# Optimization experiments

Hardware: AMD Instinct MI355X
Metric: run time of the kernel (lower is better)

The kernel has to match this reference:

```python
import jax, jax.numpy as jnp
import numpy as np

N, E, G = 50000, 200000, 1000
EPS = 1e-5
NEG_SLOPE = 0.2


def setup_inputs() -> dict:
    key = jax.random.key(0)
    ks = jax.random.split(key, 24)
    p = lambda k, shape: jax.random.normal(k, shape, jnp.float32) * 0.05
    inp = {
        "x": jax.random.normal(ks[0], (N, 64), jnp.float32),
        "edge_index": jax.random.randint(ks[1], (2, E), 0, N, jnp.int32),
        "batch": jnp.sort(jax.random.randint(ks[2], (N,), 0, G, jnp.int32)),
        "solvent_fingerprint": jax.random.uniform(ks[3], (G, 128), jnp.float32),
        # GAT layer 1: 64 -> 4 heads x 128
        "W1": p(ks[4], (64, 512)), "a1_src": p(ks[5], (4, 128)), "a1_dst": p(ks[6], (4, 128)), "b1": jnp.zeros((512,), jnp.float32),
        "bn1_g": jnp.ones((512,), jnp.float32), "bn1_b": jnp.zeros((512,), jnp.float32),
        # GAT layer 2: 512 -> 4 heads x 256
        "W2": p(ks[7], (512, 1024)), "a2_src": p(ks[8], (4, 256)), "a2_dst": p(ks[9], (4, 256)), "b2": jnp.zeros((1024,), jnp.float32),
        "bn2_g": jnp.ones((1024,), jnp.float32), "bn2_b": jnp.zeros((1024,), jnp.float32),
        # GCN: 1024 -> 256
        "Wg": p(ks[10], (1024, 256)), "bg": jnp.zeros((256,), jnp.float32),
        "bn3_g": jnp.ones((256,), jnp.float32), "bn3_b": jnp.zeros((256,), jnp.float32),
        # MLP head
        "Ws": p(ks[11], (128, 128)), "bs": jnp.zeros((128,), jnp.float32),
        "Wf1": p(ks[12], (640, 128)), "bf1": jnp.zeros((128,), jnp.float32),
        "bnf_g": jnp.ones((128,), jnp.float32), "bnf_b": jnp.zeros((128,), jnp.float32),
        "Wf2": p(ks[13], (128, 1)), "bf2": jnp.zeros((1,), jnp.float32),
    }
    return inp


def _batchnorm(x, g, b):
    mu = x.mean(0)
    var = x.var(0)
    return (x - mu) * jax.lax.rsqrt(var + EPS) * g + b


def _gat(x, src, dst, W, a_src, a_dst, b, H, C):
    n = x.shape[0]
    h = (x @ W).reshape(n, H, C)                      # [N,H,C]
    al_s = (h * a_src).sum(-1)                        # [N,H]
    al_d = (h * a_dst).sum(-1)                        # [N,H]
    e = jax.nn.leaky_relu(al_s[src] + al_d[dst], NEG_SLOPE)   # [E,H]
    m = jax.ops.segment_max(e, dst, num_segments=n)
    ex = jnp.exp(e - m[dst])
    s = jax.ops.segment_sum(ex, dst, num_segments=n)
    alpha = ex / jnp.maximum(s[dst], 1e-16)
    out = jax.ops.segment_sum(h[src] * alpha[..., None], dst, num_segments=n)  # [N,H,C]
    return out.reshape(n, H * C) + b


def _gcn(x, src, dst, W, b):
    n = x.shape[0]
    h = x @ W
    deg = jax.ops.segment_sum(jnp.ones_like(dst, jnp.float32), dst, num_segments=n)
    dinv = jax.lax.rsqrt(jnp.maximum(deg, 1.0))
    norm = dinv[src] * dinv[dst]
    return jax.ops.segment_sum(h[src] * norm[:, None], dst, num_segments=n) + b


def reference(x, edge_index, batch, solvent_fingerprint,
              W1, a1_src, a1_dst, b1, bn1_g, bn1_b,
              W2, a2_src, a2_dst, b2, bn2_g, bn2_b,
              Wg, bg, bn3_g, bn3_b,
              Ws, bs, Wf1, bf1, bnf_g, bnf_b, Wf2, bf2):
    n = x.shape[0]
    loops = jnp.arange(n, dtype=edge_index.dtype)
    src = jnp.concatenate([edge_index[0], loops])
    dst = jnp.concatenate([edge_index[1], loops])

    h = _gat(x, src, dst, W1, a1_src, a1_dst, b1, 4, 128)
    h = jax.nn.relu(_batchnorm(h, bn1_g, bn1_b))
    h = _gat(h, src, dst, W2, a2_src, a2_dst, b2, 4, 256)
    h = jax.nn.relu(_batchnorm(h, bn2_g, bn2_b))
    h = _gcn(h, src, dst, Wg, bg)
    h = jax.nn.relu(_batchnorm(h, bn3_g, bn3_b))

    cnt = jax.ops.segment_sum(jnp.ones((n,), jnp.float32), batch, num_segments=G)
    gap = jax.ops.segment_sum(h, batch, num_segments=G) / jnp.maximum(cnt, 1.0)[:, None]
    gmp = jax.ops.segment_max(h, batch, num_segments=G)
    gmp = jnp.where(jnp.isfinite(gmp), gmp, 0.0)

    solv = jax.nn.relu(solvent_fingerprint @ Ws + bs)
    z = jnp.concatenate([gap, gmp, solv], axis=1)          # [G,640]
    z = jax.nn.relu(_batchnorm(z @ Wf1 + bf1, bnf_g, bnf_b))
    # dropout: identity in eval/deterministic reference
    return jax.nn.sigmoid(z @ Wf2 + bf2)
```

## Files before the change

### kernel.cpp

```cpp
#include <hip/hip_runtime.h>
#include <cmath>

#define LEAK 0.2f
#define BN_EPS 1e-5f

static inline int cdiv(long long a, long long b){ return (int)((a + b - 1) / b); }

typedef __attribute__((ext_vector_type(8))) short bf16x8;
typedef __attribute__((ext_vector_type(4))) float f32x4;

__device__ __forceinline__ float bf2f(unsigned short u){
    return __uint_as_float(((unsigned int)u) << 16);
}
__device__ __forceinline__ unsigned short f2bf(float f){
    unsigned int u = __float_as_uint(f);
    u += 0x7FFFu + ((u >> 16) & 1u);
    return (unsigned short)(u >> 16);
}
__device__ __forceinline__ float edge_ex(float s, float d){
    float t = s + d;
    t = (t >= 0.f) ? t : LEAK * t;
    return __expf(t);
}

#define GLOAD_LDS16(gsrc, ldst) \
    __builtin_amdgcn_global_load_lds( \
        (const __attribute__((address_space(1))) unsigned int*)(gsrc), \
        (__attribute__((address_space(3))) unsigned int*)(ldst), 16, 0, 0)

__global__ __launch_bounds__(256) void gemm_mfma(
    const unsigned short* __restrict__ A, const unsigned short* __restrict__ Bt,
    unsigned short* __restrict__ D, int M, int K, int lda, int ldb, int ldc,
    int NX, int NYT, float* __restrict__ ps, float* __restrict__ pq, int Dbn,
    int axoff)
{
    const int id = blockIdx.x;
    const int xcd = id & 7;
    const int j = id >> 3;
    const int bx = j % NX;
    const int by = (j / NX) * 8 + xcd;
    if (by >= NYT) return;

    __shared__ unsigned short As[128 * 64];
    __shared__ unsigned short Bs[128 * 64];
    const int t = threadIdx.x;
    const int row0 = by * 128, col0 = bx * 128;
    const int lane = t & 63, wv = t >> 6;
    const int wm = (wv >> 1) << 6, wn = (wv & 1) << 6;
    const int lm = lane & 15, lq = lane >> 4;

    const unsigned short* Ab = A + (size_t)bx * axoff;
    const int sr  = t >> 3;
    const int scs = (t & 7) << 3;
    const int gsw = (((t & 7) ^ (sr & 7)) << 3);
    const unsigned short* ap[4];
    const unsigned short* bp[4];
    unsigned short* la[4];
    unsigned short* lb[4];
    #pragma unroll
    for (int q = 0; q < 4; ++q) {
        int r = sr + q * 32;
        int gra = row0 + r; if (gra >= M) gra = M - 1;
        ap[q] = Ab + (size_t)gra * lda + gsw;
        bp[q] = Bt + (size_t)(col0 + r) * ldb + gsw;
        la[q] = &As[r * 64 + scs];
        lb[q] = &Bs[r * 64 + scs];
    }

    f32x4 acc[4][4] = {};
    const int rx = lm & 7;

    for (int k0 = 0; k0 < K; k0 += 64) {
        #pragma unroll
        for (int q = 0; q < 4; ++q) {
            GLOAD_LDS16(ap[q] + k0, la[q]);
            GLOAD_LDS16(bp[q] + k0, lb[q]);
        }
        __syncthreads();

        #pragma unroll
        for (int kk = 0; kk < 2; ++kk) {
            const int ck = (((kk << 2) + lq) ^ rx) << 3;
            bf16x8 af[4], bfr[4];
            #pragma unroll
            for (int mi = 0; mi < 4; ++mi)
                af[mi] = *(const bf16x8*)&As[(wm + mi * 16 + lm) * 64 + ck];
            #pragma unroll
            for (int ni = 0; ni < 4; ++ni)
                bfr[ni] = *(const bf16x8*)&Bs[(wn + ni * 16 + lm) * 64 + ck];
            #pragma unroll
            for (int mi = 0; mi < 4; ++mi)
                #pragma unroll
                for (int ni = 0; ni < 4; ++ni)
                    acc[mi][ni] = __builtin_amdgcn_mfma_f32_16x16x32_bf16(
                        af[mi], bfr[ni], acc[mi][ni], 0, 0, 0);
        }
        __syncthreads();
    }

    #pragma unroll
    for (int mi = 0; mi < 4; ++mi) {
        #pragma unroll
        for (int r = 0; r < 4; ++r) {
            int row = wm + mi * 16 + lq * 4 + r;
            unsigned short* base = (row < 64) ? &As[row * 128] : &Bs[(row - 64) * 128];
            #pragma unroll
            for (int ni = 0; ni < 4; ++ni) {
                int col = (wn + ni * 16 + lm) ^ (lq << 4);
                base[col] = f2bf(acc[mi][ni][r]);
            }
        }
    }
    __syncthreads();
    #pragma unroll
    for (int i = 0; i < 8; ++i) {
        int idx = i * 256 + t;
        int row = idx >> 4;
        int lqr = (row >> 2) & 3;
        int c8l = (idx & 15) << 3;
        int c8p = c8l ^ (lqr << 4);
        int grow = row0 + row;
        if (grow < M) {
            const unsigned short* base = (row < 64) ? &As[row * 128] : &Bs[(row - 64) * 128];
            bf16x8 v = *(const bf16x8*)&base[c8p];
            *(bf16x8*)(D + (size_t)grow * ldc + col0 + c8l) = v;
        }
    }

    if (ps) {
        float cs[4] = {}, cq[4] = {};
        #pragma unroll
        for (int mi = 0; mi < 4; ++mi) {
            int row_b = row0 + wm + mi * 16 + lq * 4;
            #pragma unroll
            for (int ni = 0; ni < 4; ++ni)
                #pragma unroll
                for (int r = 0; r < 4; ++r)
                    if (row_b + r < M) {
                        float v = acc[mi][ni][r];
                        cs[ni] += v; cq[ni] += v * v;
                    }
        }
        #pragma unroll
        for (int ni = 0; ni < 4; ++ni) {
            cs[ni] += __shfl_xor(cs[ni], 16); cs[ni] += __shfl_xor(cs[ni], 32);
            cq[ni] += __shfl_xor(cq[ni], 16); cq[ni] += __shfl_xor(cq[ni], 32);
        }
        if (lane < 16) {
            size_t slot = (size_t)(blockIdx.x & 255) * Dbn + col0;
            #pragma unroll
            for (int ni = 0; ni < 4; ++ni) {
                int c = wn + ni * 16 + lane;
                atomicAdd(&ps[slot + c], cs[ni]);
                atomicAdd(&pq[slot + c], cq[ni]);
            }
        }
    }
}

__global__ __launch_bounds__(256) void logits_valu(
    const unsigned short* __restrict__ A, const unsigned short* __restrict__ vat,
    float* __restrict__ C, int M, int K)
{
    __shared__ unsigned short vs[8 * 512];
    const int t = threadIdx.x;
    for (int i = t; i < K; i += 256)
        *(bf16x8*)&vs[i * 8] = *(const bf16x8*)(vat + (size_t)i * 8);
    __syncthreads();

    const int lane = t & 63;
    const int w = blockIdx.x * 4 + (t >> 6);
    const int Gl = K >> 3;
    const int rpw = 64 / Gl;
    const int sub = lane / Gl;
    const int li = lane - sub * Gl;
    long long row = (long long)w * rpw + sub;
    if (row >= M) return;

    bf16x8 hv = *(const bf16x8*)(A + row * K + li * 8);
    float hf[8];
    #pragma unroll
    for (int j = 0; j < 8; ++j) hf[j] = bf2f((unsigned short)hv[j]);

    float s[8];
    #pragma unroll
    for (int o = 0; o < 8; ++o) {
        bf16x8 v = *(const bf16x8*)&vs[o * K + li * 8];
        float acc = 0.f;
        #pragma unroll
        for (int j = 0; j < 8; ++j) acc += hf[j] * bf2f((unsigned short)v[j]);
        s[o] = acc;
    }
    for (int off = Gl >> 1; off; off >>= 1) {
        #pragma unroll
        for (int o = 0; o < 8; ++o) s[o] += __shfl_xor(s[o], off);
    }
    #pragma unroll
    for (int o = 0; o < 8; ++o)
        if (li == o) C[row * 8 + o] = s[o];
}

__global__ __launch_bounds__(256) void bn_apply_logits512(
    const unsigned short* __restrict__ g1b,
    const float* __restrict__ scale, const float* __restrict__ shift,
    const unsigned short* __restrict__ vat,
    unsigned short* __restrict__ o1n, float* __restrict__ C, int M, int nblk)
{
    __shared__ unsigned short vs[8 * 512];
    const int t = threadIdx.x;
    for (int i = t; i < 512; i += 256)
        *(bf16x8*)&vs[i * 8] = *(const bf16x8*)(vat + (size_t)i * 8);
    __syncthreads();

    const int lane = t & 63;
    const long long stride = (long long)nblk * 4;
    for (long long row = (long long)blockIdx.x * 4 + (t >> 6); row < M; row += stride) {
        bf16x8 u = *(const bf16x8*)(g1b + row * 512 + lane * 8);
        float4 sc0 = *(const float4*)(scale + lane * 8);
        float4 sc1 = *(const float4*)(scale + lane * 8 + 4);
        float4 sh0 = *(const float4*)(shift + lane * 8);
        float4 sh1 = *(const float4*)(shift + lane * 8 + 4);
        float hf[8];
        hf[0] = fmaxf(bf2f((unsigned short)u[0]) * sc0.x + sh0.x, 0.f);
        hf[1] = fmaxf(bf2f((unsigned short)u[1]) * sc0.y + sh0.y, 0.f);
        hf[2] = fmaxf(bf2f((unsigned short)u[2]) * sc0.z + sh0.z, 0.f);
        hf[3] = fmaxf(bf2f((unsigned short)u[3]) * sc0.w + sh0.w, 0.f);
        hf[4] = fmaxf(bf2f((unsigned short)u[4]) * sc1.x + sh1.x, 0.f);
        hf[5] = fmaxf(bf2f((unsigned short)u[5]) * sc1.y + sh1.y, 0.f);
        hf[6] = fmaxf(bf2f((unsigned short)u[6]) * sc1.z + sh1.z, 0.f);
        hf[7] = fmaxf(bf2f((unsigned short)u[7]) * sc1.w + sh1.w, 0.f);
        bf16x8 o;
        #pragma unroll
        for (int j = 0; j < 8; ++j) o[j] = (short)f2bf(hf[j]);
        *(bf16x8*)(o1n + row * 512 + lane * 8) = o;

        float s[8];
        #pragma unroll
        for (int oo = 0; oo < 8; ++oo) {
            bf16x8 v = *(const bf16x8*)&vs[oo * 512 + lane * 8];
            float acc = 0.f;
            #pragma unroll
            for (int j = 0; j < 8; ++j) acc += hf[j] * bf2f((unsigned short)v[j]);
            s[oo] = acc;
        }
        #pragma unroll
        for (int off = 32; off; off >>= 1) {
            #pragma unroll
            for (int oo = 0; oo < 8; ++oo) s[oo] += __shfl_xor(s[oo], off);
        }
        #pragma unroll
        for (int oo = 0; oo < 8; ++oo)
            if (lane == oo) C[row * 8 + oo] = s[oo];
    }
}

__global__ __launch_bounds__(256) void prep_all(
    const float* __restrict__ W1, const float* __restrict__ W2,
    const float* __restrict__ Wg, const float* __restrict__ x,
    const float* __restrict__ a1s, const float* __restrict__ a1d,
    const float* __restrict__ a2s, const float* __restrict__ a2d,
    const int* __restrict__ batch,
    unsigned short* __restrict__ W1ct, unsigned short* __restrict__ W2t,
    unsigned short* __restrict__ Wgt, unsigned short* __restrict__ xb,
    unsigned short* __restrict__ vat1, unsigned short* __restrict__ vat2,
    int* __restrict__ cursor, int* __restrict__ gptr,
    int N, int G_,
    int c0, int c1, int c2, int c3, int c4, int c5, int c6)
{
    const int t = threadIdx.x;
    const int bid = blockIdx.x;
    if (bid < c0) {
        int i = bid * 256 + t;
        int o = i >> 6, k = i & 63;
        W1ct[i] = f2bf(W1[(size_t)k * 512 + o]);
    } else if (bid < c1) {
        int i = (bid - c0) * 256 + t;
        int k = i >> 10, n = i & 1023;
        W2t[(size_t)n * 512 + k] = f2bf(W2[i]);
    } else if (bid < c2) {
        int i = (bid - c1) * 256 + t;
        int k = i >> 8, n = i & 255;
        Wgt[(size_t)n * 1024 + k] = f2bf(Wg[i]);
    } else if (bid < c3) {
        int i = (bid - c2) * 256 + t;
        if (i < N * 16) {
            float4 v = *reinterpret_cast<const float4*>(x + (size_t)i * 4);
            ushort4 o = { f2bf(v.x), f2bf(v.y), f2bf(v.z), f2bf(v.w) };
            *reinterpret_cast<ushort4*>(xb + (size_t)i * 4) = o;
        }
    } else if (bid < c4) {
        int w = (((bid - c3) * 256 + t) >> 6);
        int lane = t & 63;
        int k = w >> 2, h = w & 3;
        const float* wp = W1 + (size_t)k * 512 + h * 128;
        const float* as = a1s + h * 128;
        const float* ad = a1d + h * 128;
        float s = 0.f, d = 0.f;
        for (int c = lane; c < 128; c += 64) {
            float v = wp[c];
            s += v * as[c];
            d += v * ad[c];
        }
        #pragma unroll
        for (int off = 32; off; off >>= 1) {
            s += __shfl_down(s, off);
            d += __shfl_down(d, off);
        }
        if (lane == 0) {
            vat1[(size_t)h * 64 + k] = f2bf(s);
            vat1[(size_t)(4 + h) * 64 + k] = f2bf(d);
        }
    } else if (bid < c5) {
        int w = (((bid - c4) * 256 + t) >> 6);
        int lane = t & 63;
        int k = w >> 2, h = w & 3;
        const float* wp = W2 + (size_t)k * 1024 + h * 256;
        const float* as = a2s + h * 256;
        const float* ad = a2d + h * 256;
        float s = 0.f, d = 0.f;
        for (int c = lane; c < 256; c += 64) {
            float v = wp[c];
            s += v * as[c];
            d += v * ad[c];
        }
        #pragma unroll
        for (int off = 32; off; off >>= 1) {
            s += __shfl_down(s, off);
            d += __shfl_down(d, off);
        }
        if (lane == 0) {
            vat2[(size_t)h * 512 + k] = f2bf(s);
            vat2[(size_t)(4 + h) * 512 + k] = f2bf(d);
        }
    } else if (bid < c6) {
        int i = (bid - c5) * 256 + t;
        if (i < N) cursor[i] = 1;
    } else {
        int g = (bid - c6) * 256 + t;
        if (g > G_) return;
        if (g == G_) { gptr[G_] = N; return; }
        int lo = 0, hi = N;
        while (lo < hi) { int mid = (lo + hi) >> 1; if (batch[mid] < g) lo = mid + 1; else hi = mid; }
        gptr[g] = lo;
    }
}

template<bool RELU>
__global__ __launch_bounds__(256) void gemm_small(
    const float* __restrict__ A, const float* __restrict__ B,
    const float* __restrict__ bias, float* __restrict__ C,
    int M, int K, int lda, int ldb, int ldc,
    float* __restrict__ ps, float* __restrict__ pq)
{
    __shared__ float As[2][640];
    const int t = threadIdx.x;
    const int r = t >> 7, c = t & 127;
    const int row0 = blockIdx.x * 2;
    for (int i = t; i < 2 * K; i += 256) {
        int rr = i / K, kk = i - rr * K;
        int gr = row0 + rr;
        As[rr][kk] = (gr < M) ? A[(size_t)gr * lda + kk] : 0.f;
    }
    __syncthreads();
    float acc0 = 0.f, acc1 = 0.f;
    for (int k = 0; k < K; k += 8) {
        float4 a0 = *reinterpret_cast<const float4*>(&As[r][k]);
        float4 a1 = *reinterpret_cast<const float4*>(&As[r][k + 4]);
        acc0 += a0.x * B[(size_t)(k + 0) * ldb + c];
        acc1 += a0.y * B[(size_t)(k + 1) * ldb + c];
        acc0 += a0.z * B[(size_t)(k + 2) * ldb + c];
        acc1 += a0.w * B[(size_t)(k + 3) * ldb + c];
        acc0 += a1.x * B[(size_t)(k + 4) * ldb + c];
        acc1 += a1.y * B[(size_t)(k + 5) * ldb + c];
        acc0 += a1.z * B[(size_t)(k + 6) * ldb + c];
        acc1 += a1.w * B[(size_t)(k + 7) * ldb + c];
    }
    int row = row0 + r;
    if (row < M) {
        float v = acc0 + acc1;
        if (bias) v += bias[c];
        if (RELU) v = fmaxf(v, 0.f);
        C[(size_t)row * ldc + c] = v;
        if (ps) {
            size_t slot = (size_t)(blockIdx.x & 255) * 128 + c;
            atomicAdd(&ps[slot], v);
            atomicAdd(&pq[slot], v * v);
        }
    }
}

__device__ __forceinline__ int e_src(const int* es, int E, int k){ return k < E ? es[k] : k - E; }
__device__ __forceinline__ int e_dst(const int* ed, int E, int k){ return k < E ? ed[k] : k - E; }

__global__ void hist_dst(const int* __restrict__ ed, int E, int* __restrict__ cnt)
{
    int k = blockIdx.x * blockDim.x + threadIdx.x;
    if (k < E) atomicAdd(&cnt[ed[k]], 1);
}

__global__ __launch_bounds__(256) void scan_blk(const int* __restrict__ cnt,
                                                int* __restrict__ rowptr,
                                                int* __restrict__ bsums, int n)
{
    __shared__ int ts[256];
    const int t = threadIdx.x;
    const int i0 = blockIdx.x * 1024 + t * 4;
    int4 v = {0, 0, 0, 0};
    if (i0 + 3 < n) v = *reinterpret_cast<const int4*>(cnt + i0);
    else {
        if (i0 + 0 < n) v.x = cnt[i0 + 0];
        if (i0 + 1 < n) v.y = cnt[i0 + 1];
        if (i0 + 2 < n) v.z = cnt[i0 + 2];
        if (i0 + 3 < n) v.w = cnt[i0 + 3];
    }
    int lsum = v.x + v.y + v.z + v.w;
    ts[t] = lsum;
    __syncthreads();
    #pragma unroll
    for (int off = 1; off < 256; off <<= 1) {
        int u = (t >= off) ? ts[t - off] : 0;
        __syncthreads();
        ts[t] += u;
        __syncthreads();
    }
    int excl = ts[t] - lsum;
    if (i0 + 0 < n) rowptr[i0 + 0] = excl;
    if (i0 + 1 < n) rowptr[i0 + 1] = excl + v.x;
    if (i0 + 2 < n) rowptr[i0 + 2] = excl + v.x + v.y;
    if (i0 + 3 < n) rowptr[i0 + 3] = excl + v.x + v.y + v.z;
    if (t == 255) bsums[blockIdx.x] = ts[255];
}

__global__ __launch_bounds__(256) void scan_tops(int* __restrict__ bsums,
                                                 int* __restrict__ rowptr, int nb, int n)
{
    __shared__ int ts[256];
    const int t = threadIdx.x;
    int v = (t < nb) ? bsums[t] : 0;
    ts[t] = v;
    __syncthreads();
    #pragma unroll
    for (int off = 1; off < 256; off <<= 1) {
        int u = (t >= off) ? ts[t - off] : 0;
        __syncthreads();
        ts[t] += u;
        __syncthreads();
    }
    if (t < nb) bsums[t] = ts[t] - v;
    if (t == 255) rowptr[n] = ts[255];
}

__global__ void scan_add(int* __restrict__ rowptr, int* __restrict__ cursor,
                         const int* __restrict__ bsums, int n)
{
    int i = blockIdx.x * blockDim.x + threadIdx.x;
    if (i >= n) return;
    int r = rowptr[i] + bsums[i >> 10];
    rowptr[i] = r;
    cursor[i] = r;
}

__global__ void csr_scatter_dinv(const int* __restrict__ es, const int* __restrict__ ed,
                                 int E, int Etot, int* __restrict__ cursor,
                                 int* __restrict__ col,
                                 const int* __restrict__ rowptr,
                                 float* __restrict__ dinv, int N, int NBsc)
{
    const int bid = blockIdx.x;
    const int t = threadIdx.x;
    if (bid < NBsc) {
        int k = bid * 256 + t;
        if (k >= Etot) return;
        int sn = e_src(es, E, k), dn = e_dst(ed, E, k);
        int pos = atomicAdd(&cursor[dn], 1);
        col[pos] = sn;
    } else {
        int i = (bid - NBsc) * 256 + t;
        if (i < N) dinv[i] = rsqrtf(fmaxf((float)(rowptr[i + 1] - rowptr[i]), 1.f));
    }
}

__global__ void gat_agg4_64(const int* __restrict__ rowptr, const int* __restrict__ col,
                            const unsigned short* __restrict__ xb,
                            const float* __restrict__ alsd,
                            unsigned short* __restrict__ agg, int N)
{
    int w = (int)(((long long)blockIdx.x * blockDim.x + threadIdx.x) >> 6);
    int lane = threadIdx.x & 63;
    if (w >= N) return;
    float4 dt = *reinterpret_cast<const float4*>(alsd + (size_t)w * 8 + 4);
    int r0 = rowptr[w], r1 = rowptr[w + 1];
    float a0 = 0.f, a1 = 0.f, a2 = 0.f, a3 = 0.f;
    float s0 = 0.f, s1 = 0.f, s2 = 0.f, s3 = 0.f;
    int e = r0;
    for (; e + 1 < r1; e += 2) {
        int snA = col[e], snB = col[e + 1];
        float4 stA = *reinterpret_cast<const float4*>(alsd + (size_t)snA * 8);
        float4 stB = *reinterpret_cast<const float4*>(alsd + (size_t)snB * 8);
        float xA = bf2f(xb[(size_t)snA * 64 + lane]);
        float xB = bf2f(xb[(size_t)snB * 64 + lane]);
        float eA0 = edge_ex(stA.x, dt.x), eB0 = edge_ex(stB.x, dt.x);
        float eA1 = edge_ex(stA.y, dt.y), eB1 = edge_ex(stB.y, dt.y);
        float eA2 = edge_ex(stA.z, dt.z), eB2 = edge_ex(stB.z, dt.z);
        float eA3 = edge_ex(stA.w, dt.w), eB3 = edge_ex(stB.w, dt.w);
        a0 += eA0 * xA + eB0 * xB;  s0 += eA0 + eB0;
        a1 += eA1 * xA + eB1 * xB;  s1 += eA1 + eB1;
        a2 += eA2 * xA + eB2 * xB;  s2 += eA2 + eB2;
        a3 += eA3 * xA + eB3 * xB;  s3 += eA3 + eB3;
    }
    if (e < r1) {
        int sn = col[e];
        float4 st = *reinterpret_cast<const float4*>(alsd + (size_t)sn * 8);
        float xA = bf2f(xb[(size_t)sn * 64 + lane]);
        float e0 = edge_ex(st.x, dt.x);
        float e1 = edge_ex(st.y, dt.y);
        float e2 = edge_ex(st.z, dt.z);
        float e3 = edge_ex(st.w, dt.w);
        a0 += e0 * xA; s0 += e0;
        a1 += e1 * xA; s1 += e1;
        a2 += e2 * xA; s2 += e2;
        a3 += e3 * xA; s3 += e3;
    }
    unsigned short* op = agg + (size_t)w * 256 + lane;
    op[0]   = f2bf(a0 / fmaxf(s0, 1e-16f));
    op[64]  = f2bf(a1 / fmaxf(s1, 1e-16f));
    op[128] = f2bf(a2 / fmaxf(s2, 1e-16f));
    op[192] = f2bf(a3 / fmaxf(s3, 1e-16f));
}

__global__ __launch_bounds__(256) void gat_gather512_ex(
    const int* __restrict__ rowptr, const int* __restrict__ col,
    const unsigned short* __restrict__ h, int ldh,
    const float* __restrict__ alsd, int pr,
    unsigned short* __restrict__ out,
    float* __restrict__ ps, float* __restrict__ pq, int N)
{
    const int t = threadIdx.x;
    const int lane = t & 63;
    const int wv = t >> 6;
    int w = (int)(((long long)blockIdx.x * 256 + t) >> 6);
    const bool valid = (w < N);

    float v0=0.f,v1=0.f,v2=0.f,v3=0.f;
    float u0=0.f,u1=0.f,u2=0.f,u3=0.f;
    if (valid) {
        float2 dt = *reinterpret_cast<const float2*>(alsd + (size_t)w * 8 + 4 + 2 * pr);
        int r0 = rowptr[w], r1 = rowptr[w + 1];
        float s0 = 0.f, s1 = 0.f;
        float a00=0.f,a01=0.f,a02=0.f,a03=0.f;
        float a10=0.f,a11=0.f,a12=0.f,a13=0.f;
        int e = r0;
        for (; e + 1 < r1; e += 2) {
            int snA = col[e], snB = col[e + 1];
            float2 stA = *reinterpret_cast<const float2*>(alsd + (size_t)snA * 8 + 2 * pr);
            float2 stB = *reinterpret_cast<const float2*>(alsd + (size_t)snB * 8 + 2 * pr);
            const unsigned short* pA = h + (size_t)snA * ldh + lane * 4;
            const unsigned short* pB = h + (size_t)snB * ldh + lane * 4;
            ushort4 hA0 = *reinterpret_cast<const ushort4*>(pA);
            ushort4 hA1 = *reinterpret_cast<const ushort4*>(pA + 256);
            ushort4 hB0 = *reinterpret_cast<const ushort4*>(pB);
            ushort4 hB1 = *reinterpret_cast<const ushort4*>(pB + 256);
            float eA0 = edge_ex(stA.x, dt.x), eB0 = edge_ex(stB.x, dt.x);
            float eA1 = edge_ex(stA.y, dt.y), eB1 = edge_ex(stB.y, dt.y);
            s0 += eA0 + eB0; s1 += eA1 + eB1;
            a00 += bf2f(hA0.x) * eA0 + bf2f(hB0.x) * eB0;
            a01 += bf2f(hA0.y) * eA0 + bf2f(hB0.y) * eB0;
            a02 += bf2f(hA0.z) * eA0 + bf2f(hB0.z) * eB0;
            a03 += bf2f(hA0.w) * eA0 + bf2f(hB0.w) * eB0;
            a10 += bf2f(hA1.x) * eA1 + bf2f(hB1.x) * eB1;
            a11 += bf2f(hA1.y) * eA1 + bf2f(hB1.y) * eB1;
            a12 += bf2f(hA1.z) * eA1 + bf2f(hB1.z) * eB1;
            a13 += bf2f(hA1.w) * eA1 + bf2f(hB1.w) * eB1;
        }
        if (e < r1) {
            int sn = col[e];
            float2 st = *reinterpret_cast<const float2*>(alsd + (size_t)sn * 8 + 2 * pr);
            float e0 = edge_ex(st.x, dt.x);
            float e1 = edge_ex(st.y, dt.y);
            const unsigned short* p = h + (size_t)sn * ldh + lane * 4;
            ushort4 h0 = *reinterpret_cast<const ushort4*>(p);
            ushort4 h1 = *reinterpret_cast<const ushort4*>(p + 256);
            s0 += e0; s1 += e1;
            a00 += bf2f(h0.x) * e0; a01 += bf2f(h0.y) * e0;
            a02 += bf2f(h0.z) * e0; a03 += bf2f(h0.w) * e0;
            a10 += bf2f(h1.x) * e1; a11 += bf2f(h1.y) * e1;
            a12 += bf2f(h1.z) * e1; a13 += bf2f(h1.w) * e1;
        }
        float i0 = 1.f / fmaxf(s0, 1e-16f);
        float i1 = 1.f / fmaxf(s1, 1e-16f);
        v0 = a00*i0; v1 = a01*i0; v2 = a02*i0; v3 = a03*i0;
        u0 = a10*i1; u1 = a11*i1; u2 = a12*i1; u3 = a13*i1;
        ushort4 o0 = { f2bf(v0), f2bf(v1), f2bf(v2), f2bf(v3) };
        ushort4 o1 = { f2bf(u0), f2bf(u1), f2bf(u2), f2bf(u3) };
        unsigned short* op = out + (size_t)w * 512 + lane * 4;
        *reinterpret_cast<ushort4*>(op)       = o0;
        *reinterpret_cast<ushort4*>(op + 256) = o1;
    }

    __shared__ float ls[4][512];
    __shared__ float lq[4][512];
    int c0 = lane * 4;
    ls[wv][c0+0]=v0; ls[wv][c0+1]=v1; ls[wv][c0+2]=v2; ls[wv][c0+3]=v3;
    ls[wv][256+c0+0]=u0; ls[wv][256+c0+1]=u1; ls[wv][256+c0+2]=u2; ls[wv][256+c0+3]=u3;
    lq[wv][c0+0]=v0*v0; lq[wv][c0+1]=v1*v1; lq[wv][c0+2]=v2*v2; lq[wv][c0+3]=v3*v3;
    lq[wv][256+c0+0]=u0*u0; lq[wv][256+c0+1]=u1*u1; lq[wv][256+c0+2]=u2*u2; lq[wv][256+c0+3]=u3*u3;
    __syncthreads();
    const size_t slot = (size_t)(blockIdx.x & 255) * 512;
    #pragma unroll
    for (int c = t; c < 512; c += 256) {
        float s = ls[0][c] + ls[1][c] + ls[2][c] + ls[3][c];
        float q = lq[0][c] + lq[1][c] + lq[2][c] + lq[3][c];
        atomicAdd(&ps[slot + c], s);
        atomicAdd(&pq[slot + c], q);
    }
}

__global__ __launch_bounds__(256) void gcn_gather256(
    const int* __restrict__ rowptr, const int* __restrict__ col,
    const unsigned short* __restrict__ h,
    const float* __restrict__ dinv,
    unsigned short* __restrict__ out,
    float* __restrict__ ps, float* __restrict__ pq, int N)
{
    const int t = threadIdx.x;
    const int lane = t & 63;
    const int wv = t >> 6;
    int w = (int)(((long long)blockIdx.x * 256 + t) >> 6);
    const bool valid = (w < N);

    float v0=0.f,v1=0.f,v2=0.f,v3=0.f;
    if (valid) {
        int r0 = rowptr[w], r1 = rowptr[w + 1];
        float a0 = 0.f, a1 = 0.f, a2 = 0.f, a3 = 0.f;
        int e = r0;
        for (; e + 1 < r1; e += 2) {
            int sn0 = col[e], sn1 = col[e + 1];
            float w0 = dinv[sn0], w1 = dinv[sn1];
            ushort4 hv0 = *reinterpret_cast<const ushort4*>(h + (size_t)sn0 * 256 + lane * 4);
            ushort4 hv1 = *reinterpret_cast<const ushort4*>(h + (size_t)sn1 * 256 + lane * 4);
            a0 += bf2f(hv0.x) * w0 + bf2f(hv1.x) * w1;
            a1 += bf2f(hv0.y) * w0 + bf2f(hv1.y) * w1;
            a2 += bf2f(hv0.z) * w0 + bf2f(hv1.z) * w1;
            a3 += bf2f(hv0.w) * w0 + bf2f(hv1.w) * w1;
        }
        if (e < r1) {
            int sn = col[e];
            float wv2 = dinv[sn];
            ushort4 hv = *reinterpret_cast<const ushort4*>(h + (size_t)sn * 256 + lane * 4);
            a0 += bf2f(hv.x) * wv2; a1 += bf2f(hv.y) * wv2;
            a2 += bf2f(hv.z) * wv2; a3 += bf2f(hv.w) * wv2;
        }
        float dn = dinv[w];
        v0 = a0 * dn; v1 = a1 * dn; v2 = a2 * dn; v3 = a3 * dn;
        ushort4 o = { f2bf(v0), f2bf(v1), f2bf(v2), f2bf(v3) };
        *reinterpret_cast<ushort4*>(out + (size_t)w * 256 + lane * 4) = o;
    }

    __shared__ float ls[4][256];
    __shared__ float lq[4][256];
    int c0 = lane * 4;
    ls[wv][c0+0]=v0; ls[wv][c0+1]=v1; ls[wv][c0+2]=v2; ls[wv][c0+3]=v3;
    lq[wv][c0+0]=v0*v0; lq[wv][c0+1]=v1*v1; lq[wv][c0+2]=v2*v2; lq[wv][c0+3]=v3*v3;
    __syncthreads();
    const size_t slot = (size_t)(blockIdx.x & 255) * 256;
    if (t < 256) {
        int c = t;
        float s = ls[0][c] + ls[1][c] + ls[2][c] + ls[3][c];
        float q = lq[0][c] + lq[1][c] + lq[2][c] + lq[3][c];
        atomicAdd(&ps[slot + c], s);
        atomicAdd(&pq[slot + c], q);
    }
}

template<int D>
__global__ __launch_bounds__(256) void bn_reduce_fin(
    const float* __restrict__ ps, const float* __restrict__ pq,
    const float* __restrict__ g, const float* __restrict__ b,
    float* __restrict__ scale, float* __restrict__ shift, int Y, float invM)
{
    const int t = threadIdx.x;
    const int cl = t & 63;
    const int c = blockIdx.x * 64 + cl;
    const int ph = t >> 6;
    float s = 0.f, q = 0.f;
    for (int y = ph; y < Y; y += 4) {
        s += ps[(size_t)y * D + c];
        q += pq[(size_t)y * D + c];
    }
    __shared__ float ls[4][64];
    __shared__ float lq[4][64];
    ls[ph][cl] = s; lq[ph][cl] = q;
    __syncthreads();
    if (ph == 0) {
        s = ls[0][cl] + ls[1][cl] + ls[2][cl] + ls[3][cl];
        q = lq[0][cl] + lq[1][cl] + lq[2][cl] + lq[3][cl];
        float mu = s * invM;
        float var = q * invM - mu * mu;
        float rs = rsqrtf(var + BN_EPS) * g[c];
        scale[c] = rs;
        shift[c] = b[c] - mu * rs;
    }
}

__global__ void bn_apply_bfbf(const unsigned short* __restrict__ x,
                              const float* __restrict__ scale, const float* __restrict__ shift,
                              unsigned short* __restrict__ dst, int total4, int Cb4,
                              int ldx, int ldd)
{
    int i = blockIdx.x * blockDim.x + threadIdx.x;
    if (i >= total4) return;
    int r = i / Cb4, c4 = (i - r * Cb4) * 4;
    ushort4 u = *reinterpret_cast<const ushort4*>(x + (size_t)r * ldx + c4);
    float4 sc = *reinterpret_cast<const float4*>(scale + c4);
    float4 sh = *reinterpret_cast<const float4*>(shift + c4);
    ushort4 o;
    o.x = f2bf(fmaxf(bf2f(u.x) * sc.x + sh.x, 0.f));
    o.y = f2bf(fmaxf(bf2f(u.y) * sc.y + sh.y, 0.f));
    o.z = f2bf(fmaxf(bf2f(u.z) * sc.z + sh.z, 0.f));
    o.w = f2bf(fmaxf(bf2f(u.w) * sc.w + sh.w, 0.f));
    *reinterpret_cast<ushort4*>(dst + (size_t)r * ldd + c4) = o;
}

__global__ __launch_bounds__(256) void pool_solv(
    const unsigned short* __restrict__ h,
    const float* __restrict__ scale, const float* __restrict__ shift,
    const int* __restrict__ gptr, float* __restrict__ z, int G_,
    const float* __restrict__ sfp, const float* __restrict__ Wsm,
    const float* __restrict__ bsm)
{
    __shared__ float As[2][640];
    const int t = threadIdx.x;
    const int bid = blockIdx.x;
    if (bid < G_) {
        int g = bid;
        int c = t;
        int r0 = gptr[g], r1 = gptr[g + 1];
        float sc = scale[c], sh = shift[c];
        float s = 0.f, m = 0.f;
        int i = r0;
        for (; i + 1 < r1; i += 2) {
            float v0 = fmaxf(bf2f(h[(size_t)i * 256 + c]) * sc + sh, 0.f);
            float v1 = fmaxf(bf2f(h[(size_t)(i + 1) * 256 + c]) * sc + sh, 0.f);
            s += v0 + v1;
            m = fmaxf(m, fmaxf(v0, v1));
        }
        if (i < r1) {
            float v = fmaxf(bf2f(h[(size_t)i * 256 + c]) * sc + sh, 0.f);
            s += v;
            m = fmaxf(m, v);
        }
        float cnt = fmaxf((float)(r1 - r0), 1.f);
        z[(size_t)g * 640 + c] = s / cnt;
        z[(size_t)g * 640 + 256 + c] = m;
    } else {
        const int r = t >> 7, c = t & 127;
        const int row0 = (bid - G_) * 2;
        for (int i = t; i < 256; i += 256) {
            int rr = i >> 7, kk = i & 127;
            int gr = row0 + rr;
            As[rr][kk] = (gr < G_) ? sfp[(size_t)gr * 128 + kk] : 0.f;
        }
        __syncthreads();
        float acc0 = 0.f, acc1 = 0.f;
        for (int k = 0; k < 128; k += 8) {
            float4 a0 = *reinterpret_cast<const float4*>(&As[r][k]);
            float4 a1 = *reinterpret_cast<const float4*>(&As[r][k + 4]);
            acc0 += a0.x * Wsm[(size_t)(k + 0) * 128 + c];
            acc1 += a0.y * Wsm[(size_t)(k + 1) * 128 + c];
            acc0 += a0.z * Wsm[(size_t)(k + 2) * 128 + c];
            acc1 += a0.w * Wsm[(size_t)(k + 3) * 128 + c];
            acc0 += a1.x * Wsm[(size_t)(k + 4) * 128 + c];
            acc1 += a1.y * Wsm[(size_t)(k + 5) * 128 + c];
            acc0 += a1.z * Wsm[(size_t)(k + 6) * 128 + c];
            acc1 += a1.w * Wsm[(size_t)(k + 7) * 128 + c];
        }
        int row = row0 + r;
        if (row < G_) {
            float v = fmaxf(acc0 + acc1 + bsm[c], 0.f);
            z[(size_t)row * 640 + 512 + c] = v;
        }
    }
}

__global__ void final_head_bn(const float* __restrict__ f1,
                              const float* __restrict__ scale, const float* __restrict__ shift,
                              const float* __restrict__ Wf2, const float* __restrict__ bf2,
                              float* __restrict__ out, int G_)
{
    int w = (int)(((long long)blockIdx.x * blockDim.x + threadIdx.x) >> 6);
    int lane = threadIdx.x & 63;
    if (w >= G_) return;
    float s = 0.f;
    #pragma unroll
    for (int q = 0; q < 2; ++q) {
        int c = lane + q * 64;
        float v = fmaxf(f1[(size_t)w * 128 + c] * scale[c] + shift[c], 0.f);
        s += v * Wf2[c];
    }
    #pragma unroll
    for (int off = 32; off; off >>= 1) s += __shfl_down(s, off);
    if (lane == 0) out[w] = 1.f / (1.f + __expf(-(s + bf2[0])));
}

__global__ void sentinel(float* __restrict__ out, int n, float v)
{
    int i = blockIdx.x * blockDim.x + threadIdx.x;
    if (i < n) out[i] = v;
}

extern "C" void kernel_launch(void* const* d_in, const int* in_sizes, int n_in,
                              void* d_out, int out_size, void* d_ws, size_t ws_size,
                              hipStream_t stream)
{
    const float* x    = (const float*)d_in[0];
    const int*   ei   = (const int*)d_in[1];
    const int*   batch= (const int*)d_in[2];
    const float* sfp  = (const float*)d_in[3];
    const float* W1   = (const float*)d_in[4];
    const float* a1s  = (const float*)d_in[5];
    const float* a1d  = (const float*)d_in[6];
    const float* bn1g = (const float*)d_in[8];
    const float* bn1b = (const float*)d_in[9];
    const float* W2   = (const float*)d_in[10];
    const float* a2s  = (const float*)d_in[11];
    const float* a2d  = (const float*)d_in[12];
    const float* bn2g = (const float*)d_in[14];
    const float* bn2b = (const float*)d_in[15];
    const float* Wg   = (const float*)d_in[16];
    const float* bn3g = (const float*)d_in[18];
    const float* bn3b = (const float*)d_in[19];
    const float* Wsm  = (const float*)d_in[20];
    const float* bsm  = (const float*)d_in[21];
    const float* Wf1  = (const float*)d_in[22];
    const float* bnfg = (const float*)d_in[24];
    const float* bnfb = (const float*)d_in[25];
    const float* Wf2  = (const float*)d_in[26];
    const float* bf2  = (const float*)d_in[27];
    float* outp = (float*)d_out;

    const int N    = in_sizes[0] / 64;
    const int E    = in_sizes[1] / 2;
    const int G_   = in_sizes[3] / 128;
    const int Etot = E + N;
    const int* esrc = ei;
    const int* edst = ei + E;
    const int YB = 256;
    const int NB = cdiv(N, 1024);
    const int NYT = cdiv(N, 128);
    const int NYT8 = cdiv(NYT, 8) * 8;

    float* ws = (float*)d_ws;
    size_t off = 0;
    float* accA  = ws + off; off += (size_t)N * 256;
    float* h3acc = ws + off; off += (size_t)N * 256;
    unsigned short* g1b   = (unsigned short*)accA;
    unsigned short* g3b   = (unsigned short*)accA;
    unsigned short* h2all = (unsigned short*)accA;
    unsigned short* R1 = (unsigned short*)(ws + off); off += (size_t)N * 256;
    unsigned short* o1n = R1;
    unsigned short* hb  = (unsigned short*)(ws + off); off += (size_t)N * 128;
    unsigned short* xb  = (unsigned short*)(ws + off); off += (size_t)N * 32;
    float* alsd = ws + off; off += (size_t)N * 8;
    float* dinv = ws + off; off += N;
    float* bsc = ws + off; off += 1024;
    float* bsh = ws + off; off += 1024;
    float* ps  = ws + off; off += (size_t)YB * 1920;
    float* pq  = ws + off; off += (size_t)YB * 1920;
    float* psP0 = ps + (size_t)YB * 512;
    float* psP1 = ps + (size_t)YB * 1024;
    float* psG  = ps + (size_t)YB * 1536;
    float* psF  = ps + (size_t)YB * 1792;
    float* pqP0 = pq + (size_t)YB * 512;
    float* pqP1 = pq + (size_t)YB * 1024;
    float* pqG  = pq + (size_t)YB * 1536;
    float* pqF  = pq + (size_t)YB * 1792;
    float* z   = ws + off; off += (size_t)G_ * 640;
    float* f1  = ws + off; off += (size_t)G_ * 128;
    int* rowptr = (int*)(ws + off); off += (size_t)(N + 1);
    int* colc   = (int*)(ws + off); off += (size_t)Etot;
    int* gptr   = (int*)(ws + off); off += (size_t)(G_ + 1);
    int* bsums  = (int*)(ws + off); off += 256;
    off = (off + 3) & ~(size_t)3;
    unsigned short* vat1 = (unsigned short*)(ws + off); off += 128 * 64 / 2;
    unsigned short* vat2 = (unsigned short*)(ws + off); off += 128 * 512 / 2;
    unsigned short* W1ct = (unsigned short*)(ws + off); off += 512 * 64 / 2;
    unsigned short* W2t = (unsigned short*)(ws + off); off += 512 * 1024 / 2;
    unsigned short* Wgt = (unsigned short*)(ws + off); off += 1024 * 256 / 2;
    int* cursor = (int*)alsd;
    size_t need = off * 4;
    if (ws_size < need) {
        sentinel<<<cdiv(out_size, 256), 256, 0, stream>>>(outp, out_size, (float)(ws_size >> 20));
        return;
    }

    const int BLK = 256;
    dim3 blk(BLK);

    hipMemsetAsync(ps, 0, (size_t)YB * 1920 * 4, stream);
    hipMemsetAsync(pq, 0, (size_t)YB * 1920 * 4, stream);

    const int c0 = 128;
    const int c1 = c0 + 2048;
    const int c2 = c1 + 1024;
    const int c3 = c2 + cdiv((long long)N * 16, 256);
    const int c4 = c3 + 64;
    const int c5 = c4 + 512;
    const int c6 = c5 + cdiv(N, 256);
    const int c7 = c6 + cdiv(G_ + 1, 256);
    prep_all<<<c7, blk, 0, stream>>>(W1, W2, Wg, x, a1s, a1d, a2s, a2d, batch,
                                     W1ct, W2t, Wgt, xb, vat1, vat2,
                                     cursor, gptr, N, G_,
                                     c0, c1, c2, c3, c4, c5, c6);

    hist_dst<<<cdiv(E, BLK), blk, 0, stream>>>(edst, E, cursor);
    scan_blk<<<NB, blk, 0, stream>>>(cursor, rowptr, bsums, N);
    scan_tops<<<1, blk, 0, stream>>>(bsums, rowptr, NB, N);
    scan_add<<<cdiv(N, BLK), blk, 0, stream>>>(rowptr, cursor, bsums, N);
    { int NBsc = cdiv(Etot, BLK);
      csr_scatter_dinv<<<NBsc + cdiv(N, BLK), blk, 0, stream>>>(
          esrc, edst, E, Etot, cursor, colc, rowptr, dinv, N, NBsc); }

    logits_valu<<<cdiv(N, 32), blk, 0, stream>>>(xb, vat1, alsd, N, 64);
    gat_agg4_64<<<cdiv((long long)N * 64, BLK), blk, 0, stream>>>(
        rowptr, colc, xb, alsd, hb, N);
    gemm_mfma<<<NYT8 * 4, blk, 0, stream>>>(hb, W1ct, g1b, N, 64, 256, 64, 512, 4, NYT,
                                            ps, pq, 512, 64);
    bn_reduce_fin<512><<<8, blk, 0, stream>>>(ps, pq, bn1g, bn1b, bsc, bsh, YB, 1.f / N);
    bn_apply_logits512<<<2048, blk, 0, stream>>>(
        g1b, bsc, bsh, vat2, o1n, alsd, N, 2048);

    gemm_mfma<<<NYT8 * 8, blk, 0, stream>>>(o1n, W2t, h2all, N, 512, 512, 512, 1024, 8, NYT,
                                            nullptr, nullptr, 0, 0);
    for (int pr = 0; pr < 2; ++pr) {
        float* pssite = pr ? psP1 : psP0;
        float* pqsite = pr ? pqP1 : pqP0;
        gat_gather512_ex<<<cdiv((long long)N * 64, BLK), blk, 0, stream>>>(
            rowptr, colc, h2all + pr * 512, 1024, alsd, pr, R1, pssite, pqsite, N);
        bn_reduce_fin<512><<<8, blk, 0, stream>>>(pssite, pqsite, bn2g + pr * 512, bn2b + pr * 512,
                                                  bsc + pr * 512, bsh + pr * 512, YB, 1.f / N);
        bn_apply_bfbf<<<cdiv((long long)N * 128, BLK), blk, 0, stream>>>(
            R1, bsc + pr * 512, bsh + pr * 512, h2all + pr * 512, N * 128, 128, 512, 1024);
    }

    gemm_mfma<<<NYT8 * 2, blk, 0, stream>>>(h2all, Wgt, hb, N, 1024, 1024, 1024, 256, 2, NYT,
                                            nullptr, nullptr, 0, 0);

    gcn_gather256<<<cdiv((long long)N * 64, BLK), blk, 0, stream>>>(
        rowptr, colc, hb, dinv, g3b, psG, pqG, N);
    bn_reduce_fin<256><<<4, blk, 0, stream>>>(psG, pqG, bn3g, bn3b, bsc, bsh, YB, 1.f / N);

    pool_solv<<<G_ + cdiv(G_, 2), blk, 0, stream>>>(
        g3b, bsc, bsh, gptr, z, G_, sfp, Wsm, bsm);

    gemm_small<false><<<cdiv(G_, 2), blk, 0, stream>>>(
        z, Wf1, nullptr, f1, G_, 640, 640, 128, 128, psF, pqF);
    bn_reduce_fin<128><<<2, blk, 0, stream>>>(psF, pqF, bnfg, bnfb, bsc, bsh, YB, 1.f / G_);
    final_head_bn<<<cdiv((long long)G_ * 64, BLK), blk, 0, stream>>>(
        f1, bsc, bsh, Wf2, bf2, outp, G_);
}
```

Before: 718.0 us.

## Fuse two half-width GAT layer-2 gathers into one full-width 1024-column pass

Replaces the two sequential 512-column attention gather passes (each with its own BN reduce and apply) with a single kernel that aggregates all 1024 columns per destination node. The edge list, attention logits and exponentials are read and computed once instead of twice, and the launch count drops. In exchange it needs an extra N×1024 bf16 scratch buffer, more registers per thread and 32KB of shared memory per block. It falls back to the old path if the workspace is too small.

New measurement: 722.2 us. About the same (+0.6%).

```diff
diff --git a/kernel.cpp b/kernel.cpp
--- a/kernel.cpp
+++ b/kernel.cpp
@@ -526,6 +526,99 @@
     op[64]  = f2bf(a1 / fmaxf(s1, 1e-16f));
     op[128] = f2bf(a2 / fmaxf(s2, 1e-16f));
     op[192] = f2bf(a3 / fmaxf(s3, 1e-16f));
+}
+
+__global__ __launch_bounds__(256) void gat_gather1024(
+    const int* __restrict__ rowptr, const int* __restrict__ col,
+    const unsigned short* __restrict__ h,
+    const float* __restrict__ alsd,
+    unsigned short* __restrict__ out,
+    float* __restrict__ ps, float* __restrict__ pq, int N)
+{
+    const int t = threadIdx.x;
+    const int lane = t & 63;
+    const int wv = t >> 6;
+    int w = (int)(((long long)blockIdx.x * 256 + t) >> 6);
+    const bool valid = (w < N);
+
+    float v[4][4] = {};
+    if (valid) {
+        float4 dt = *reinterpret_cast<const float4*>(alsd + (size_t)w * 8 + 4);
+        int r0 = rowptr[w], r1 = rowptr[w + 1];
+        float sm[4] = {};
+        float a[4][4] = {};
+        int e = r0;
+        for (; e + 1 < r1; e += 2) {
+            int snA = col[e], snB = col[e + 1];
+            float4 stA = *reinterpret_cast<const float4*>(alsd + (size_t)snA * 8);
+            float4 stB = *reinterpret_cast<const float4*>(alsd + (size_t)snB * 8);
+            const unsigned short* pA = h + (size_t)snA * 1024 + lane * 4;
+            const unsigned short* pB = h + (size_t)snB * 1024 + lane * 4;
+            float eA[4], eB[4];
+            eA[0] = edge_ex(stA.x, dt.x); eB[0] = edge_ex(stB.x, dt.x);
+            eA[1] = edge_ex(stA.y, dt.y); eB[1] = edge_ex(stB.y, dt.y);
+            eA[2] = edge_ex(stA.z, dt.z); eB[2] = edge_ex(stB.z, dt.z);
+            eA[3] = edge_ex(stA.w, dt.w); eB[3] = edge_ex(stB.w, dt.w);
+            #pragma unroll
+            for (int s = 0; s < 4; ++s) {
+                ushort4 hA = *reinterpret_cast<const ushort4*>(pA + s * 256);
+                ushort4 hB = *reinterpret_cast<const ushort4*>(pB + s * 256);
+                sm[s] += eA[s] + eB[s];
+                a[s][0] += bf2f(hA.x) * eA[s] + bf2f(hB.x) * eB[s];
+                a[s][1] += bf2f(hA.y) * eA[s] + bf2f(hB.y) * eB[s];
+                a[s][2] += bf2f(hA.z) * eA[s] + bf2f(hB.z) * eB[s];
+                a[s][3] += bf2f(hA.w) * eA[s] + bf2f(hB.w) * eB[s];
+            }
+        }
+        if (e < r1) {
+            int sn = col[e];
+            float4 st = *reinterpret_cast<const float4*>(alsd + (size_t)sn * 8);
+            const unsigned short* p = h + (size_t)sn * 1024 + lane * 4;
+            float ee[4];
+            ee[0] = edge_ex(st.x, dt.x);
+            ee[1] = edge_ex(st.y, dt.y);
+            ee[2] = edge_ex(st.z, dt.z);
+            ee[3] = edge_ex(st.w, dt.w);
+            #pragma unroll
+            for (int s = 0; s < 4; ++s) {
+                ushort4 hv = *reinterpret_cast<const ushort4*>(p + s * 256);
+                sm[s] += ee[s];
+                a[s][0] += bf2f(hv.x) * ee[s];
+                a[s][1] += bf2f(hv.y) * ee[s];
+                a[s][2] += bf2f(hv.z) * ee[s];
+                a[s][3] += bf2f(hv.w) * ee[s];
+            }
+        }
+        unsigned short* op = out + (size_t)w * 1024 + lane * 4;
+        #pragma unroll
+        for (int s = 0; s < 4; ++s) {
+            float inv = 1.f / fmaxf(sm[s], 1e-16f);
+            v[s][0] = a[s][0] * inv; v[s][1] = a[s][1] * inv;
+            v[s][2] = a[s][2] * inv; v[s][3] = a[s][3] * inv;
+            ushort4 o = { f2bf(v[s][0]), f2bf(v[s][1]), f2bf(v[s][2]), f2bf(v[s][3]) };
+            *reinterpret_cast<ushort4*>(op + s * 256) = o;
+        }
+    }
+
+    __shared__ float ls[4][1024];
+    __shared__ float lq[4][1024];
+    #pragma unroll
+    for (int s = 0; s < 4; ++s) {
+        int c0 = s * 256 + lane * 4;
+        ls[wv][c0+0] = v[s][0]; ls[wv][c0+1] = v[s][1];
+        ls[wv][c0+2] = v[s][2]; ls[wv][c0+3] = v[s][3];
+        lq[wv][c0+0] = v[s][0]*v[s][0]; lq[wv][c0+1] = v[s][1]*v[s][1];
+        lq[wv][c0+2] = v[s][2]*v[s][2]; lq[wv][c0+3] = v[s][3]*v[s][3];
+    }
+    __syncthreads();
+    const size_t slot = (size_t)(blockIdx.x & 255) * 1024;
+    #pragma unroll
+    for (int c = t; c < 1024; c += 256) {
+        float s = ls[0][c] + ls[1][c] + ls[2][c] + ls[3][c];
+        float q = lq[0][c] + lq[1][c] + lq[2][c] + lq[3][c];
+        atomicAdd(&ps[slot + c], s);
+        atomicAdd(&pq[slot + c], q);
+    }
 }
 
 __global__ __launch_bounds__(256) void gat_gather512_ex(
@@ -888,6 +981,9 @@
     unsigned short* Wgt = (unsigned short*)(ws + off); off += 1024 * 256 / 2;
     int* cursor = (int*)alsd;
     size_t need = off * 4;
+    unsigned short* R2 = (unsigned short*)(ws + off);
+    size_t need_r2 = (off + (size_t)N * 512) * 4;
+    const bool merged = (ws_size >= need_r2);
     if (ws_size < need) {
         sentinel<<<cdiv(out_size, 256), 256, 0, stream>>>(outp, out_size, (float)(ws_size >> 20));
         return;
@@ -931,15 +1027,25 @@
 
     gemm_mfma<<<NYT8 * 8, blk, 0, stream>>>(o1n, W2t, h2all, N, 512, 512, 512, 1024, 8, NYT,
                                             nullptr, nullptr, 0, 0);
-    for (int pr = 0; pr < 2; ++pr) {
-        float* pssite = pr ? psP1 : psP0;
-        float* pqsite = pr ? pqP1 : pqP0;
-        gat_gather512_ex<<<cdiv((long long)N * 64, BLK), blk, 0, stream>>>(
-            rowptr, colc, h2all + pr * 512, 1024, alsd, pr, R1, pssite, pqsite, N);
-        bn_reduce_fin<512><<<8, blk, 0, stream>>>(pssite, pqsite, bn2g + pr * 512, bn2b + pr * 512,
-                                                  bsc + pr * 512, bsh + pr * 512, YB, 1.f / N);
-        bn_apply_bfbf<<<cdiv((long long)N * 128, BLK), blk, 0, stream>>>(
-            R1, bsc + pr * 512, bsh + pr * 512, h2all + pr * 512, N * 128, 128, 512, 1024);
+    if (merged) {
+        gat_gather1024<<<cdiv((long long)N * 64, BLK), blk, 0, stream>>>(
+            rowptr, colc, h2all, alsd, R2, psP0, pqP0, N);
+        bn_reduce_fin<1024><<<16, blk, 0, stream>>>(psP0, pqP0, bn2g, bn2b,
+                                                    bsc, bsh, YB, 1.f / N);
+        bn_apply_bfbf<<<cdiv((long long)N * 256, BLK), blk, 0, stream>>>(
+            R2, bsc, bsh, h2all, N * 256, 256, 1024, 1024);
+    } else {
+        for (int pr = 0; pr < 2; ++pr) {
+            float* pssite = pr ? psP1 : psP0;
+            float* pqsite = pr ? pqP1 : pqP0;
+            gat_gather512_ex<<<cdiv((long long)N * 64, BLK), blk, 0, stream>>>(
+                rowptr, colc, h2all + pr * 512, 1024, alsd, pr, R1, pssite, pqsite, N);
+            bn_reduce_fin<512><<<8, blk, 0, stream>>>(pssite, pqsite, bn2g + pr * 512,
+                                                      bn2b + pr * 512,
+                                                      bsc + pr * 512, bsh + pr * 512, YB, 1.f / N);
+            bn_apply_bfbf<<<cdiv((long long)N * 128, BLK), blk, 0, stream>>>(
+                R1, bsc + pr * 512, bsh + pr * 512, h2all + pr * 512, N * 128, 128, 512, 1024);
+        }
     }
 
     gemm_mfma<<<NYT8 * 2, blk, 0, stream>>>(h2all, Wgt, hb, N, 1024, 1024, 1024, 256, 2, NYT,
```
